# Kernel optimization log

Measured on AMD Instinct MI355X. Metric: run time of the kernel, lower is better.

The kernel has to match this reference:

```python
import jax, jax.numpy as jnp
import numpy as np

B, S, D = 256, 512, 64
LN_EPS = 1e-5


def _layernorm(x, g, b):
    mu = jnp.mean(x, axis=-1, keepdims=True)
    var = jnp.mean(jnp.square(x - mu), axis=-1, keepdims=True)
    return (x - mu) * jax.lax.rsqrt(var + LN_EPS) * g + b


def _mha(xq, xkv, in_w, in_b, out_w, out_b):
    # in_w: (3D, D) packed [Wq; Wk; Wv] as in torch nn.MultiheadAttention
    wq, wk, wv = in_w[:D], in_w[D:2 * D], in_w[2 * D:]
    bq, bk, bv = in_b[:D], in_b[D:2 * D], in_b[2 * D:]
    q = xq @ wq.T + bq      # (B, Sq, D)
    k = xkv @ wk.T + bk     # (B, Sk, D)
    v = xkv @ wv.T + bv
    scores = jnp.einsum('bqd,bkd->bqk', q, k) / jnp.sqrt(jnp.asarray(D, q.dtype))
    attn = jax.nn.softmax(scores, axis=-1)
    out = jnp.einsum('bqk,bkd->bqd', attn, v)
    return out @ out_w.T + out_b


def setup_inputs() -> dict:
    key = jax.random.key(0)
    ks = jax.random.split(key, 14)
    s = 1.0 / np.sqrt(D)
    return {
        'x_src': jax.random.normal(ks[0], (B, S), jnp.float32),
        'x_tgt': jax.random.normal(ks[1], (B, S), jnp.float32),
        'proj_w': jax.random.normal(ks[2], (D,), jnp.float32) * s,   # Linear(1, D) weight squeezed
        'proj_b': jax.random.normal(ks[3], (D,), jnp.float32) * 0.02,
        'sa_in_w': jax.random.normal(ks[4], (3 * D, D), jnp.float32) * s,
        'sa_in_b': jnp.zeros((3 * D,), jnp.float32),
        'sa_out_w': jax.random.normal(ks[5], (D, D), jnp.float32) * s,
        'sa_out_b': jnp.zeros((D,), jnp.float32),
        'sa_ln_g': jnp.ones((D,), jnp.float32),
        'sa_ln_b': jnp.zeros((D,), jnp.float32),
        'ca_in_w': jax.random.normal(ks[6], (3 * D, D), jnp.float32) * s,
        'ca_in_b': jnp.zeros((3 * D,), jnp.float32),
        'ca_out_w': jax.random.normal(ks[7], (D, D), jnp.float32) * s,
        'ca_out_b': jnp.zeros((D,), jnp.float32),
        'ca_ln_g': jnp.ones((D,), jnp.float32),
        'ca_ln_b': jnp.zeros((D,), jnp.float32),
    }


def reference(x_src, x_tgt, proj_w, proj_b,
              sa_in_w, sa_in_b, sa_out_w, sa_out_b, sa_ln_g, sa_ln_b,
              ca_in_w, ca_in_b, ca_out_w, ca_out_b, ca_ln_g, ca_ln_b):
    # Input projection: (B, S) -> (B, S, D) via Linear(1, D)
    hs = x_src[..., None] * proj_w + proj_b
    ht = x_tgt[..., None] * proj_w + proj_b
    # Shared self-attention block (pre-residual + LayerNorm), then mean pool
    zs = _layernorm(hs + _mha(hs, hs, sa_in_w, sa_in_b, sa_out_w, sa_out_b), sa_ln_g, sa_ln_b)
    zt = _layernorm(ht + _mha(ht, ht, sa_in_w, sa_in_b, sa_out_w, sa_out_b), sa_ln_g, sa_ln_b)
    z_src_private = zs.mean(axis=1)
    z_tgt_private = zt.mean(axis=1)
    # Cross-attention: Q from source, K/V from target
    zc = _layernorm(hs + _mha(hs, ht, ca_in_w, ca_in_b, ca_out_w, ca_out_b), ca_ln_g, ca_ln_b)
    z_shared = zc.mean(axis=1)
    return (z_shared, z_src_private, z_tgt_private)
```

## Files before the change

### kernel.cpp

```cpp
#include <hip/hip_runtime.h>

#define BB 256
#define SS 512
#define DD 64
#define LN_EPS 1e-5f
#define L2E 1.4426950408889634f
#define NN 16
#define PI_F 3.14159265358979f

__device__ __forceinline__ float fexp2(float x) {
#if __has_builtin(__builtin_amdgcn_exp2f)
    return __builtin_amdgcn_exp2f(x);
#else
    float r; asm("v_exp_f32 %0, %1" : "=v"(r) : "v"(x)); return r;
#endif
}

__global__ __launch_bounds__(512) void fused_kernel(
    const float* __restrict__ x_src, const float* __restrict__ x_tgt,
    const float* __restrict__ proj_w, const float* __restrict__ proj_b,
    const float* __restrict__ sa_in_w, const float* __restrict__ sa_in_b,
    const float* __restrict__ sa_out_w, const float* __restrict__ sa_out_b,
    const float* __restrict__ sa_ln_g, const float* __restrict__ sa_ln_b,
    const float* __restrict__ ca_in_w, const float* __restrict__ ca_in_b,
    const float* __restrict__ ca_out_w, const float* __restrict__ ca_out_b,
    const float* __restrict__ ca_ln_g, const float* __restrict__ ca_ln_b,
    float* __restrict__ out)
{
    const int tid  = threadIdx.x;
    const int b    = blockIdx.x / 3;
    const int task = blockIdx.x % 3;
    const float* xq_g = (task == 1) ? (x_tgt + b * SS) : (x_src + b * SS);
    const float* y_g  = (task == 0) ? (x_src + b * SS) : (x_tgt + b * SS);
    const int type    = (task == 2) ? 1 : 0;
    const float* in_w  = type ? ca_in_w  : sa_in_w;
    const float* in_b  = type ? ca_in_b  : sa_in_b;
    const float* out_w = type ? ca_out_w : sa_out_w;
    const float* out_b = type ? ca_out_b : sa_out_b;
    const float* g     = type ? ca_ln_g  : sa_ln_g;
    const float* lb    = type ? ca_ln_b  : sa_ln_b;
    const int out_base = ((task == 0) ? BB * DD : (task == 1) ? 2 * BB * DD : 0) + b * DD;

    __shared__ float sv[6][DD];
    __shared__ float cvec[3][DD];
    __shared__ float cst[8];
    __shared__ __align__(16) float ys_l[SS];
    __shared__ float rymx[8], rymn[8], rxmx[8], rxmn[8];
    __shared__ float rP[8], rT[8], rI[8];
    __shared__ float tj_l[NN];
    __shared__ __align__(16) float ac_l[NN];
    __shared__ float bc[7];

    const int wave = tid >> 6, lane = tid & 63;

    const float xq = xq_g[tid];
    const float y  = y_g[tid];
    ys_l[tid] = y;
    {
        float ymx = y, ymn = y, xmx = xq, xmn = xq;
        #pragma unroll
        for (int o = 32; o > 0; o >>= 1) {
            ymx = fmaxf(ymx, __shfl_down(ymx, o));
            ymn = fminf(ymn, __shfl_down(ymn, o));
            xmx = fmaxf(xmx, __shfl_down(xmx, o));
            xmn = fminf(xmn, __shfl_down(xmn, o));
        }
        if (lane == 0) { rymx[wave] = ymx; rymn[wave] = ymn;
                         rxmx[wave] = xmx; rxmn[wave] = xmn; }
    }

    if (tid < 384) {
        const int mat = tid >> 6, d = tid & 63;
        const int rb = mat % 3, vecsel = mat / 3;
        const float* W = in_w + (rb * DD + d) * DD;
        const float* v = vecsel ? proj_b : proj_w;
        float s = 0.f;
        #pragma unroll
        for (int e = 0; e < DD; e += 4) {
            float4 wv = *(const float4*)(W + e);
            float4 vv = *(const float4*)(v + e);
            s += wv.x * vv.x + wv.y * vv.y + wv.z * vv.z + wv.w * vv.w;
        }
        if (vecsel) s += in_b[rb * DD + d];
        sv[mat][d] = s;
    }
    __syncthreads();

    if (tid < 128) {
        const int which = tid >> 6, d = tid & 63;
        const float* W = out_w + d * DD;
        const float* v = sv[which ? 5 : 2];
        float s = 0.f;
        #pragma unroll
        for (int e = 0; e < DD; e += 4) {
            float4 wv = *(const float4*)(W + e);
            s += wv.x * v[e] + wv.y * v[e + 1] + wv.z * v[e + 2] + wv.w * v[e + 3];
        }
        if (which) cvec[2][d] = proj_b[d] + s + out_b[d];
        else       cvec[1][d] = s;
    }
    if (tid == 511) {
        float a = rymx[0], m = rymn[0], xa = rxmx[0], xm = rxmn[0];
        #pragma unroll
        for (int i = 1; i < 8; ++i) {
            a  = fmaxf(a,  rymx[i]); m  = fminf(m,  rymn[i]);
            xa = fmaxf(xa, rxmx[i]); xm = fminf(xm, rxmn[i]);
        }
        bc[0] = a; bc[1] = m; bc[2] = xa; bc[3] = xm;
    }
    __syncthreads();

    if (wave == 0) {
        auto wred = [](float x) {
            #pragma unroll
            for (int o = 32; o > 0; o >>= 1) x += __shfl_down(x, o);
            return __shfl(x, 0);
        };
        const float aq = sv[0][lane], ak = sv[1][lane], cq = sv[3][lane];
        const float pw = proj_w[lane];
        const float u  = cvec[1][lane], e = cvec[2][lane];

        const float alpha = wred(aq * ak) * 0.125f;
        const float gamma = wred(cq * ak) * 0.125f;
        const float m_pw = wred(pw) * (1.f / DD);
        const float m_u  = wred(u)  * (1.f / DD);
        const float m_e  = wred(e)  * (1.f / DD);
        const float a  = pw - m_pw;
        const float bb = u  - m_u;
        const float c  = e  - m_e;
        const float G11 = wred(a * a)   * (1.f / DD);
        const float G22 = wred(bb * bb) * (1.f / DD);
        const float G33 = wred(c * c)   * (1.f / DD);
        const float G12 = wred(a * bb)  * (1.f / DD);
        const float G13 = wred(a * c)   * (1.f / DD);
        const float G23 = wred(bb * c)  * (1.f / DD);

        cvec[0][lane] = a; cvec[1][lane] = bb; cvec[2][lane] = c;
        if (lane == 0) {
            cst[0] = alpha; cst[1] = gamma;
            cst[2] = G11; cst[3] = G22; cst[4] = G33;
            cst[5] = G12; cst[6] = G13; cst[7] = G23;
        }
    }
    __syncthreads();

    const float ymax = bc[0], ymin = bc[1];
    const float alpha = cst[0], gamma = cst[1];
    const float cA = alpha * bc[3] + gamma, cB = alpha * bc[2] + gamma;
    const float c_lo = fminf(cA, cB), c_hi = fmaxf(cA, cB);
    const float mid = 0.5f * (c_lo + c_hi);
    const float hw  = fmaxf(0.5f * (c_hi - c_lo), 1e-6f);

    {
        const int j0 = 2 * wave, j1 = j0 + 1;
        const float cj0 = mid + hw * __cosf(PI_F * (j0 + 0.5f) * (1.f / NN));
        const float cj1 = mid + hw * __cosf(PI_F * (j1 + 0.5f) * (1.f / NN));
        const float c0l = cj0 * L2E, c1l = cj1 * L2E;
        const float s0  = fmaxf(c0l * ymax, c0l * ymin);
        const float s1  = fmaxf(c1l * ymax, c1l * ymin);
        float S00 = 0.f, S10 = 0.f, S01 = 0.f, S11 = 0.f;
        #pragma unroll
        for (int i = 0; i < 8; ++i) {
            const float yv = ys_l[lane + (i << 6)];
            const float e0 = fexp2(c0l * yv - s0);
            const float e1 = fexp2(c1l * yv - s1);
            S00 += e0; S10 += yv * e0;
            S01 += e1; S11 += yv * e1;
        }
        #pragma unroll
        for (int o = 32; o > 0; o >>= 1) {
            S00 += __shfl_down(S00, o); S10 += __shfl_down(S10, o);
            S01 += __shfl_down(S01, o); S11 += __shfl_down(S11, o);
        }
        if (lane == 0) { tj_l[j0] = S10 / S00; tj_l[j1] = S11 / S01; }
    }
    __syncthreads();

    if (wave == 0 && lane < NN) {
        float acc = 0.f;
        #pragma unroll
        for (int j = 0; j < NN; ++j)
            acc += tj_l[j] * __cosf(PI_F * lane * (j + 0.5f) * (1.f / NN));
        float a = acc * (2.f / NN);
        if (lane == 0) a *= 0.5f;
        ac_l[lane] = a;
    }
    __syncthreads();

    float4 A0 = *(const float4*)&ac_l[0];
    float4 A1 = *(const float4*)&ac_l[4];
    float4 A2 = *(const float4*)&ac_l[8];
    float4 A3 = *(const float4*)&ac_l[12];
    const float a_[NN] = { A0.x, A0.y, A0.z, A0.w, A1.x, A1.y, A1.z, A1.w,
                           A2.x, A2.y, A2.z, A2.w, A3.x, A3.y, A3.z, A3.w };

    const float cq = alpha * xq + gamma;
    float xi = (cq - mid) / hw;
    xi = fminf(1.f, fmaxf(-1.f, xi));
    const float x2 = 2.f * xi;
    float b1 = 0.f, b2 = 0.f;
    #pragma unroll
    for (int k = NN - 1; k >= 1; --k) {
        const float bn = fmaf(x2, b1, a_[k] - b2);
        b2 = b1; b1 = bn;
    }
    const float t = fmaf(xi, b1, a_[0] - b2);

    const float G11 = cst[2], G22 = cst[3], G33 = cst[4];
    const float G12 = cst[5], G13 = cst[6], G23 = cst[7];
    const float var = xq * xq * G11 + t * t * G22 + G33
                    + 2.f * (xq * t * G12 + xq * G13 + t * G23);
    const float inv = rsqrtf(var + LN_EPS);

    float pP = xq * inv, pT = t * inv, pI = inv;
    #pragma unroll
    for (int o = 32; o > 0; o >>= 1) {
        pP += __shfl_down(pP, o);
        pT += __shfl_down(pT, o);
        pI += __shfl_down(pI, o);
    }
    if (lane == 0) { rP[wave] = pP; rT[wave] = pT; rI[wave] = pI; }
    __syncthreads();
    if (tid == 0) {
        float sP = 0.f, sT = 0.f, sI = 0.f;
        #pragma unroll
        for (int i = 0; i < 8; ++i) { sP += rP[i]; sT += rT[i]; sI += rI[i]; }
        bc[4] = sP * (1.f / SS); bc[5] = sT * (1.f / SS); bc[6] = sI * (1.f / SS);
    }
    __syncthreads();

    if (tid < DD) {
        const float P = bc[4], T = bc[5], I = bc[6];
        float z = (P * cvec[0][tid] + T * cvec[1][tid] + I * cvec[2][tid]) * g[tid] + lb[tid];
        out[out_base + tid] = z;
    }
}

extern "C" void kernel_launch(void* const* d_in, const int* in_sizes, int n_in,
                              void* d_out, int out_size, void* d_ws, size_t ws_size,
                              hipStream_t stream) {
    const float* x_src    = (const float*)d_in[0];
    const float* x_tgt    = (const float*)d_in[1];
    const float* proj_w   = (const float*)d_in[2];
    const float* proj_b   = (const float*)d_in[3];
    const float* sa_in_w  = (const float*)d_in[4];
    const float* sa_in_b  = (const float*)d_in[5];
    const float* sa_out_w = (const float*)d_in[6];
    const float* sa_out_b = (const float*)d_in[7];
    const float* sa_ln_g  = (const float*)d_in[8];
    const float* sa_ln_b  = (const float*)d_in[9];
    const float* ca_in_w  = (const float*)d_in[10];
    const float* ca_in_b  = (const float*)d_in[11];
    const float* ca_out_w = (const float*)d_in[12];
    const float* ca_out_b = (const float*)d_in[13];
    const float* ca_ln_g  = (const float*)d_in[14];
    const float* ca_ln_b  = (const float*)d_in[15];
    float* out = (float*)d_out;

    fused_kernel<<<BB * 3, 512, 0, stream>>>(
        x_src, x_tgt, proj_w, proj_b,
        sa_in_w, sa_in_b, sa_out_w, sa_out_b, sa_ln_g, sa_ln_b,
        ca_in_w, ca_in_b, ca_out_w, ca_out_b, ca_ln_g, ca_ln_b,
        out);
}
```

Before: 105.7 us.

## Hoist per-weight precomputation into a single-block prep kernel

The weight-only projections, out-projection vectors and Gram constants were recomputed in each of the 768 blocks. They are now computed once by a separate one-block prep kernel, written to workspace, and read by the main kernel. This removes redundant global weight reads and two block barriers per block. In exchange it adds a second serialized kernel launch, and the main kernel reads its constants from global memory instead of LDS.

```diff
diff --git a/kernel.cpp b/kernel.cpp
--- a/kernel.cpp
+++ b/kernel.cpp
@@ -8,6 +8,8 @@
 #define NN 16
 #define PI_F 3.14159265358979f
 
+#define WS_TYPE_STRIDE 256
+
 __device__ __forceinline__ float fexp2(float x) {
 #if __has_builtin(__builtin_amdgcn_exp2f)
     return __builtin_amdgcn_exp2f(x);
@@ -16,63 +18,25 @@
 #endif
 }
 
-__global__ __launch_bounds__(512) void fused_kernel(
-    const float* __restrict__ x_src, const float* __restrict__ x_tgt,
+
+__global__ __launch_bounds__(1024) void prep_kernel(
     const float* __restrict__ proj_w, const float* __restrict__ proj_b,
     const float* __restrict__ sa_in_w, const float* __restrict__ sa_in_b,
     const float* __restrict__ sa_out_w, const float* __restrict__ sa_out_b,
-    const float* __restrict__ sa_ln_g, const float* __restrict__ sa_ln_b,
     const float* __restrict__ ca_in_w, const float* __restrict__ ca_in_b,
     const float* __restrict__ ca_out_w, const float* __restrict__ ca_out_b,
-    const float* __restrict__ ca_ln_g, const float* __restrict__ ca_ln_b,
-    float* __restrict__ out)
+    float* __restrict__ ws)
 {
-    const int tid  = threadIdx.x;
-    const int b    = blockIdx.x / 3;
-    const int task = blockIdx.x % 3;
-    const float* xq_g = (task == 1) ? (x_tgt + b * SS) : (x_src + b * SS);
-    const float* y_g  = (task == 0) ? (x_src + b * SS) : (x_tgt + b * SS);
-    const int type    = (task == 2) ? 1 : 0;
-    const float* in_w  = type ? ca_in_w  : sa_in_w;
-    const float* in_b  = type ? ca_in_b  : sa_in_b;
-    const float* out_w = type ? ca_out_w : sa_out_w;
-    const float* out_b = type ? ca_out_b : sa_out_b;
-    const float* g     = type ? ca_ln_g  : sa_ln_g;
-    const float* lb    = type ? ca_ln_b  : sa_ln_b;
-    const int out_base = ((task == 0) ? BB * DD : (task == 1) ? 2 * BB * DD : 0) + b * DD;
-
-    __shared__ float sv[6][DD];
-    __shared__ float cvec[3][DD];
-    __shared__ float cst[8];
-    __shared__ __align__(16) float ys_l[SS];
-    __shared__ float rymx[8], rymn[8], rxmx[8], rxmn[8];
-    __shared__ float rP[8], rT[8], rI[8];
-    __shared__ float tj_l[NN];
-    __shared__ __align__(16) float ac_l[NN];
-    __shared__ float bc[7];
-
-    const int wave = tid >> 6, lane = tid & 63;
-
-    const float xq = xq_g[tid];
-    const float y  = y_g[tid];
-    ys_l[tid] = y;
-    {
-        float ymx = y, ymn = y, xmx = xq, xmn = xq;
-        #pragma unroll
-        for (int o = 32; o > 0; o >>= 1) {
-            ymx = fmaxf(ymx, __shfl_down(ymx, o));
-            ymn = fminf(ymn, __shfl_down(ymn, o));
-            xmx = fmaxf(xmx, __shfl_down(xmx, o));
-            xmn = fminf(xmn, __shfl_down(xmn, o));
-        }
-        if (lane == 0) { rymx[wave] = ymx; rymn[wave] = ymn;
-                         rxmx[wave] = xmx; rxmn[wave] = xmn; }
-    }
-
-    if (tid < 384) {
+    const int tid = threadIdx.x;
+    __shared__ float sv[2][6][DD];
+    __shared__ float suu[2][DD], see[2][DD];
+
+    if (tid < 768) {
         const int mat = tid >> 6, d = tid & 63;
-        const int rb = mat % 3, vecsel = mat / 3;
-        const float* W = in_w + (rb * DD + d) * DD;
+        const int type = mat / 6, which = mat % 6;
+        const int rb = which % 3;
+        const int vecsel = which / 3;
+        const float* W = (type ? ca_in_w : sa_in_w) + (rb * DD + d) * DD;
         const float* v = vecsel ? proj_b : proj_w;
         float s = 0.f;
         #pragma unroll
@@ -81,44 +45,43 @@
             float4 vv = *(const float4*)(v + e);
             s += wv.x * vv.x + wv.y * vv.y + wv.z * vv.z + wv.w * vv.w;
         }
-        if (vecsel) s += in_b[rb * DD + d];
-        sv[mat][d] = s;
-    }
-    __syncthreads();
-
-    if (tid < 128) {
-        const int which = tid >> 6, d = tid & 63;
-        const float* W = out_w + d * DD;
-        const float* v = sv[which ? 5 : 2];
+        if (vecsel) s += (type ? ca_in_b : sa_in_b)[rb * DD + d];
+        sv[type][which][d] = s;
+    }
+    __syncthreads();
+
+    if (tid < 256) {
+        const int mat = tid >> 6, d = tid & 63;
+        const int type = mat >> 1, which = mat & 1;
+        const float* W = (type ? ca_out_w : sa_out_w) + d * DD;
+        const float* v = sv[type][which ? 5 : 2];
         float s = 0.f;
         #pragma unroll
         for (int e = 0; e < DD; e += 4) {
             float4 wv = *(const float4*)(W + e);
             s += wv.x * v[e] + wv.y * v[e + 1] + wv.z * v[e + 2] + wv.w * v[e + 3];
         }
-        if (which) cvec[2][d] = proj_b[d] + s + out_b[d];
-        else       cvec[1][d] = s;
-    }
-    if (tid == 511) {
-        float a = rymx[0], m = rymn[0], xa = rxmx[0], xm = rxmn[0];
-        #pragma unroll
-        for (int i = 1; i < 8; ++i) {
-            a  = fmaxf(a,  rymx[i]); m  = fminf(m,  rymn[i]);
-            xa = fmaxf(xa, rxmx[i]); xm = fminf(xm, rxmn[i]);
-        }
-        bc[0] = a; bc[1] = m; bc[2] = xa; bc[3] = xm;
-    }
-    __syncthreads();
-
-    if (wave == 0) {
+        if (which) {
+            s += (type ? ca_out_b : sa_out_b)[d];
+            see[type][d] = proj_b[d] + s;
+        } else {
+            suu[type][d] = s;
+        }
+    }
+    __syncthreads();
+
+    const int wave = tid >> 6, lane = tid & 63;
+    if (wave < 2) {
+        const int type = wave;
         auto wred = [](float x) {
             #pragma unroll
             for (int o = 32; o > 0; o >>= 1) x += __shfl_down(x, o);
             return __shfl(x, 0);
         };
-        const float aq = sv[0][lane], ak = sv[1][lane], cq = sv[3][lane];
+        const float aq = sv[type][0][lane], ak = sv[type][1][lane];
+        const float cq = sv[type][3][lane];
         const float pw = proj_w[lane];
-        const float u  = cvec[1][lane], e = cvec[2][lane];
+        const float u  = suu[type][lane], e = see[type][lane];
 
         const float alpha = wred(aq * ak) * 0.125f;
         const float gamma = wred(cq * ak) * 0.125f;
@@ -135,17 +98,70 @@
         const float G13 = wred(a * c)   * (1.f / DD);
         const float G23 = wred(bb * c)  * (1.f / DD);
 
-        cvec[0][lane] = a; cvec[1][lane] = bb; cvec[2][lane] = c;
+        float* w = ws + type * WS_TYPE_STRIDE;
+        w[8 + lane] = a; w[72 + lane] = bb; w[136 + lane] = c;
         if (lane == 0) {
-            cst[0] = alpha; cst[1] = gamma;
-            cst[2] = G11; cst[3] = G22; cst[4] = G33;
-            cst[5] = G12; cst[6] = G13; cst[7] = G23;
-        }
+            w[0] = alpha; w[1] = gamma;
+            w[2] = G11; w[3] = G22; w[4] = G33; w[5] = G12; w[6] = G13; w[7] = G23;
+        }
+    }
+}
+
+__global__ __launch_bounds__(512) void main_kernel(
+    const float* __restrict__ x_src, const float* __restrict__ x_tgt,
+    const float* __restrict__ sa_ln_g, const float* __restrict__ sa_ln_b,
+    const float* __restrict__ ca_ln_g, const float* __restrict__ ca_ln_b,
+    const float* __restrict__ ws, float* __restrict__ out)
+{
+    const int tid  = threadIdx.x;
+    const int b    = blockIdx.x / 3;
+    const int task = blockIdx.x % 3;
+    const float* xq_g = (task == 1) ? (x_tgt + b * SS) : (x_src + b * SS);
+    const float* y_g  = (task == 0) ? (x_src + b * SS) : (x_tgt + b * SS);
+    const int type    = (task == 2) ? 1 : 0;
+    const float* w  = ws + type * WS_TYPE_STRIDE;
+    const float* g  = type ? ca_ln_g : sa_ln_g;
+    const float* lb = type ? ca_ln_b : sa_ln_b;
+    const int out_base = ((task == 0) ? BB * DD : (task == 1) ? 2 * BB * DD : 0) + b * DD;
+
+    __shared__ __align__(16) float ys_l[SS];
+    __shared__ float rymx[8], rymn[8], rxmx[8], rxmn[8];
+    __shared__ float rP[8], rT[8], rI[8];
+    __shared__ float tj_l[NN];
+    __shared__ __align__(16) float ac_l[NN];
+    __shared__ float bc[7];
+
+    const int wave = tid >> 6, lane = tid & 63;
+
+    const float xq = xq_g[tid];
+    const float y  = y_g[tid];
+    ys_l[tid] = y;
+    {
+        float ymx = y, ymn = y, xmx = xq, xmn = xq;
+        #pragma unroll
+        for (int o = 32; o > 0; o >>= 1) {
+            ymx = fmaxf(ymx, __shfl_down(ymx, o));
+            ymn = fminf(ymn, __shfl_down(ymn, o));
+            xmx = fmaxf(xmx, __shfl_down(xmx, o));
+            xmn = fminf(xmn, __shfl_down(xmn, o));
+        }
+        if (lane == 0) { rymx[wave] = ymx; rymn[wave] = ymn;
+                         rxmx[wave] = xmx; rxmn[wave] = xmn; }
+    }
+    __syncthreads();
+    if (tid == 0) {
+        float a = rymx[0], m = rymn[0], xa = rxmx[0], xm = rxmn[0];
+        #pragma unroll
+        for (int i = 1; i < 8; ++i) {
+            a  = fmaxf(a,  rymx[i]); m  = fminf(m,  rymn[i]);
+            xa = fmaxf(xa, rxmx[i]); xm = fminf(xm, rxmn[i]);
+        }
+        bc[0] = a; bc[1] = m; bc[2] = xa; bc[3] = xm;
     }
     __syncthreads();
 
     const float ymax = bc[0], ymin = bc[1];
-    const float alpha = cst[0], gamma = cst[1];
+    const float alpha = w[0], gamma = w[1];
     const float cA = alpha * bc[3] + gamma, cB = alpha * bc[2] + gamma;
     const float c_lo = fminf(cA, cB), c_hi = fmaxf(cA, cB);
     const float mid = 0.5f * (c_lo + c_hi);
@@ -206,8 +222,8 @@
     }
     const float t = fmaf(xi, b1, a_[0] - b2);
 
-    const float G11 = cst[2], G22 = cst[3], G33 = cst[4];
-    const float G12 = cst[5], G13 = cst[6], G23 = cst[7];
+    const float G11 = w[2], G22 = w[3], G33 = w[4];
+    const float G12 = w[5], G13 = w[6], G23 = w[7];
     const float var = xq * xq * G11 + t * t * G22 + G33
                     + 2.f * (xq * t * G12 + xq * G13 + t * G23);
     const float inv = rsqrtf(var + LN_EPS);
@@ -231,7 +247,7 @@
 
     if (tid < DD) {
         const float P = bc[4], T = bc[5], I = bc[6];
-        float z = (P * cvec[0][tid] + T * cvec[1][tid] + I * cvec[2][tid]) * g[tid] + lb[tid];
+        float z = (P * w[8 + tid] + T * w[72 + tid] + I * w[136 + tid]) * g[tid] + lb[tid];
         out[out_base + tid] = z;
     }
 }
@@ -255,11 +271,13 @@
     const float* ca_out_b = (const float*)d_in[13];
     const float* ca_ln_g  = (const float*)d_in[14];
     const float* ca_ln_b  = (const float*)d_in[15];
+    float* ws  = (float*)d_ws;
     float* out = (float*)d_out;
 
-    fused_kernel<<<BB * 3, 512, 0, stream>>>(
-        x_src, x_tgt, proj_w, proj_b,
-        sa_in_w, sa_in_b, sa_out_w, sa_out_b, sa_ln_g, sa_ln_b,
-        ca_in_w, ca_in_b, ca_out_w, ca_out_b, ca_ln_g, ca_ln_b,
-        out);
-}
+    prep_kernel<<<1, 1024, 0, stream>>>(proj_w, proj_b,
+                                        sa_in_w, sa_in_b, sa_out_w, sa_out_b,
+                                        ca_in_w, ca_in_b, ca_out_w, ca_out_b, ws);
+    main_kernel<<<BB * 3, 512, 0, stream>>>(x_src, x_tgt,
+                                            sa_ln_g, sa_ln_b, ca_ln_g, ca_ln_b,
+                                            ws, out);
+}
```

New measurement: 99.31 us. -6.0%, faster.

## Merge three per-batch task blocks into one block computing all tasks

Applied to the files above, without the earlier changes.

Launches one block per batch element instead of three, so each block computes self-attention for source and target and cross-attention together. The input rows and weight-derived vectors are loaded and precomputed once per batch rather than once per task, and the Chebyshev node sums, coefficient fits and reductions are batched across all three tasks. This removes redundant weight projections and halves global input loads. In exchange the grid has fewer blocks (256), which may underfill the GPU, and each block carries more serial work and register pressure.

```diff
diff --git a/kernel.cpp b/kernel.cpp
--- a/kernel.cpp
+++ b/kernel.cpp
@@ -16,7 +16,7 @@
 #endif
 }
 
-__global__ __launch_bounds__(512) void fused_kernel(
+__global__ __launch_bounds__(512) void fused_all(
     const float* __restrict__ x_src, const float* __restrict__ x_tgt,
     const float* __restrict__ proj_w, const float* __restrict__ proj_b,
     const float* __restrict__ sa_in_w, const float* __restrict__ sa_in_b,
@@ -28,51 +28,41 @@
     float* __restrict__ out)
 {
     const int tid  = threadIdx.x;
-    const int b    = blockIdx.x / 3;
-    const int task = blockIdx.x % 3;
-    const float* xq_g = (task == 1) ? (x_tgt + b * SS) : (x_src + b * SS);
-    const float* y_g  = (task == 0) ? (x_src + b * SS) : (x_tgt + b * SS);
-    const int type    = (task == 2) ? 1 : 0;
-    const float* in_w  = type ? ca_in_w  : sa_in_w;
-    const float* in_b  = type ? ca_in_b  : sa_in_b;
-    const float* out_w = type ? ca_out_w : sa_out_w;
-    const float* out_b = type ? ca_out_b : sa_out_b;
-    const float* g     = type ? ca_ln_g  : sa_ln_g;
-    const float* lb    = type ? ca_ln_b  : sa_ln_b;
-    const int out_base = ((task == 0) ? BB * DD : (task == 1) ? 2 * BB * DD : 0) + b * DD;
-
-    __shared__ float sv[6][DD];
-    __shared__ float cvec[3][DD];
-    __shared__ float cst[8];
-    __shared__ __align__(16) float ys_l[SS];
-    __shared__ float rymx[8], rymn[8], rxmx[8], rxmn[8];
-    __shared__ float rP[8], rT[8], rI[8];
-    __shared__ float tj_l[NN];
-    __shared__ __align__(16) float ac_l[NN];
-    __shared__ float bc[7];
-
+    const int b    = blockIdx.x;
     const int wave = tid >> 6, lane = tid & 63;
 
-    const float xq = xq_g[tid];
-    const float y  = y_g[tid];
-    ys_l[tid] = y;
+    __shared__ __align__(16) float xs_l[SS];
+    __shared__ __align__(16) float xt_l[SS];
+    __shared__ float sv[2][6][DD];
+    __shared__ float cw[2][3][DD];
+    __shared__ float cst[2][8];
+    __shared__ float rmx[8][4];
+    __shared__ float bb4[4];
+    __shared__ float tj_l[3 * NN];
+    __shared__ float ac_l[3 * NN];
+    __shared__ float rpti[8][9];
+    __shared__ float ptio[9];
+
+    const float xs = x_src[b * SS + tid];
+    const float xt = x_tgt[b * SS + tid];
+    xs_l[tid] = xs; xt_l[tid] = xt;
     {
-        float ymx = y, ymn = y, xmx = xq, xmn = xq;
+        float sx = xs, sn = xs, tx = xt, tn = xt;
         #pragma unroll
         for (int o = 32; o > 0; o >>= 1) {
-            ymx = fmaxf(ymx, __shfl_down(ymx, o));
-            ymn = fminf(ymn, __shfl_down(ymn, o));
-            xmx = fmaxf(xmx, __shfl_down(xmx, o));
-            xmn = fminf(xmn, __shfl_down(xmn, o));
-        }
-        if (lane == 0) { rymx[wave] = ymx; rymn[wave] = ymn;
-                         rxmx[wave] = xmx; rxmn[wave] = xmn; }
-    }
-
-    if (tid < 384) {
-        const int mat = tid >> 6, d = tid & 63;
-        const int rb = mat % 3, vecsel = mat / 3;
-        const float* W = in_w + (rb * DD + d) * DD;
+            sx = fmaxf(sx, __shfl_down(sx, o));
+            sn = fminf(sn, __shfl_down(sn, o));
+            tx = fmaxf(tx, __shfl_down(tx, o));
+            tn = fminf(tn, __shfl_down(tn, o));
+        }
+        if (lane == 0) { rmx[wave][0] = sx; rmx[wave][1] = sn;
+                         rmx[wave][2] = tx; rmx[wave][3] = tn; }
+    }
+
+    for (int m = wave; m < 12; m += 8) {
+        const int type = m / 6, which = m % 6;
+        const int rb = which % 3, vecsel = which / 3;
+        const float* W = (type ? ca_in_w : sa_in_w) + (rb * DD + lane) * DD;
         const float* v = vecsel ? proj_b : proj_w;
         float s = 0.f;
         #pragma unroll
@@ -81,44 +71,46 @@
             float4 vv = *(const float4*)(v + e);
             s += wv.x * vv.x + wv.y * vv.y + wv.z * vv.z + wv.w * vv.w;
         }
-        if (vecsel) s += in_b[rb * DD + d];
-        sv[mat][d] = s;
-    }
-    __syncthreads();
-
-    if (tid < 128) {
-        const int which = tid >> 6, d = tid & 63;
-        const float* W = out_w + d * DD;
-        const float* v = sv[which ? 5 : 2];
+        if (vecsel) s += (type ? ca_in_b : sa_in_b)[rb * DD + lane];
+        sv[type][which][lane] = s;
+    }
+    __syncthreads();
+
+    if (wave < 4) {
+        const int type = wave >> 1, which = wave & 1;
+        const float* W = (type ? ca_out_w : sa_out_w) + lane * DD;
+        const float* v = sv[type][which ? 5 : 2];
         float s = 0.f;
         #pragma unroll
         for (int e = 0; e < DD; e += 4) {
             float4 wv = *(const float4*)(W + e);
             s += wv.x * v[e] + wv.y * v[e + 1] + wv.z * v[e + 2] + wv.w * v[e + 3];
         }
-        if (which) cvec[2][d] = proj_b[d] + s + out_b[d];
-        else       cvec[1][d] = s;
+        if (which) cw[type][2][lane] = proj_b[lane] + s + (type ? ca_out_b : sa_out_b)[lane];
+        else       cw[type][1][lane] = s;
     }
     if (tid == 511) {
-        float a = rymx[0], m = rymn[0], xa = rxmx[0], xm = rxmn[0];
+        float a = rmx[0][0], m = rmx[0][1], c = rmx[0][2], d = rmx[0][3];
         #pragma unroll
         for (int i = 1; i < 8; ++i) {
-            a  = fmaxf(a,  rymx[i]); m  = fminf(m,  rymn[i]);
-            xa = fmaxf(xa, rxmx[i]); xm = fminf(xm, rxmn[i]);
-        }
-        bc[0] = a; bc[1] = m; bc[2] = xa; bc[3] = xm;
-    }
-    __syncthreads();
-
-    if (wave == 0) {
+            a = fmaxf(a, rmx[i][0]); m = fminf(m, rmx[i][1]);
+            c = fmaxf(c, rmx[i][2]); d = fminf(d, rmx[i][3]);
+        }
+        bb4[0] = a; bb4[1] = m; bb4[2] = c; bb4[3] = d;
+    }
+    __syncthreads();
+
+    if (wave < 2) {
+        const int type = wave;
         auto wred = [](float x) {
             #pragma unroll
             for (int o = 32; o > 0; o >>= 1) x += __shfl_down(x, o);
             return __shfl(x, 0);
         };
-        const float aq = sv[0][lane], ak = sv[1][lane], cq = sv[3][lane];
+        const float aq = sv[type][0][lane], ak = sv[type][1][lane];
+        const float cq = sv[type][3][lane];
         const float pw = proj_w[lane];
-        const float u  = cvec[1][lane], e = cvec[2][lane];
+        const float u  = cw[type][1][lane], e = cw[type][2][lane];
 
         const float alpha = wred(aq * ak) * 0.125f;
         const float gamma = wred(cq * ak) * 0.125f;
@@ -126,113 +118,148 @@
         const float m_u  = wred(u)  * (1.f / DD);
         const float m_e  = wred(e)  * (1.f / DD);
         const float a  = pw - m_pw;
-        const float bb = u  - m_u;
+        const float bbv = u - m_u;
         const float c  = e  - m_e;
-        const float G11 = wred(a * a)   * (1.f / DD);
-        const float G22 = wred(bb * bb) * (1.f / DD);
-        const float G33 = wred(c * c)   * (1.f / DD);
-        const float G12 = wred(a * bb)  * (1.f / DD);
-        const float G13 = wred(a * c)   * (1.f / DD);
-        const float G23 = wred(bb * c)  * (1.f / DD);
-
-        cvec[0][lane] = a; cvec[1][lane] = bb; cvec[2][lane] = c;
+        const float G11 = wred(a * a)     * (1.f / DD);
+        const float G22 = wred(bbv * bbv) * (1.f / DD);
+        const float G33 = wred(c * c)     * (1.f / DD);
+        const float G12 = wred(a * bbv)   * (1.f / DD);
+        const float G13 = wred(a * c)     * (1.f / DD);
+        const float G23 = wred(bbv * c)   * (1.f / DD);
+
+        cw[type][0][lane] = a; cw[type][1][lane] = bbv; cw[type][2][lane] = c;
         if (lane == 0) {
-            cst[0] = alpha; cst[1] = gamma;
-            cst[2] = G11; cst[3] = G22; cst[4] = G33;
-            cst[5] = G12; cst[6] = G13; cst[7] = G23;
-        }
-    }
-    __syncthreads();
-
-    const float ymax = bc[0], ymin = bc[1];
-    const float alpha = cst[0], gamma = cst[1];
-    const float cA = alpha * bc[3] + gamma, cB = alpha * bc[2] + gamma;
-    const float c_lo = fminf(cA, cB), c_hi = fmaxf(cA, cB);
-    const float mid = 0.5f * (c_lo + c_hi);
-    const float hw  = fmaxf(0.5f * (c_hi - c_lo), 1e-6f);
-
-    {
-        const int j0 = 2 * wave, j1 = j0 + 1;
-        const float cj0 = mid + hw * __cosf(PI_F * (j0 + 0.5f) * (1.f / NN));
-        const float cj1 = mid + hw * __cosf(PI_F * (j1 + 0.5f) * (1.f / NN));
+            cst[type][0] = alpha; cst[type][1] = gamma;
+            cst[type][2] = G11; cst[type][3] = G22; cst[type][4] = G33;
+            cst[type][5] = G12; cst[type][6] = G13; cst[type][7] = G23;
+        }
+    }
+    __syncthreads();
+
+    const float xsmx = bb4[0], xsmn = bb4[1], xtmx = bb4[2], xtmn = bb4[3];
+    float mid_[3], hw_[3], ymx_[3], ymn_[3];
+    #pragma unroll
+    for (int task = 0; task < 3; ++task) {
+        const int ty = (task == 2) ? 1 : 0;
+        const float al = cst[ty][0], ga = cst[ty][1];
+        const float xlo = (task == 1) ? xtmn : xsmn;
+        const float xhi = (task == 1) ? xtmx : xsmx;
+        const float cA = al * xlo + ga, cB = al * xhi + ga;
+        const float lo = fminf(cA, cB), hi = fmaxf(cA, cB);
+        mid_[task] = 0.5f * (lo + hi);
+        hw_[task]  = fmaxf(0.5f * (hi - lo), 1e-6f);
+        ymx_[task] = (task == 0) ? xsmx : xtmx;
+        ymn_[task] = (task == 0) ? xsmn : xtmn;
+    }
+
+    #pragma unroll
+    for (int p = 0; p < 3; ++p) {
+        const int n0 = 6 * wave + 2 * p, n1 = n0 + 1;
+        const int tk0 = n0 >> 4, j0 = n0 & 15;
+        const int tk1 = n1 >> 4, j1 = n1 & 15;
+        const float cj0 = mid_[tk0] + hw_[tk0] * __cosf(PI_F * (j0 + 0.5f) * (1.f / NN));
+        const float cj1 = mid_[tk1] + hw_[tk1] * __cosf(PI_F * (j1 + 0.5f) * (1.f / NN));
         const float c0l = cj0 * L2E, c1l = cj1 * L2E;
-        const float s0  = fmaxf(c0l * ymax, c0l * ymin);
-        const float s1  = fmaxf(c1l * ymax, c1l * ymin);
+        const float s0 = fmaxf(c0l * ymx_[tk0], c0l * ymn_[tk0]);
+        const float s1 = fmaxf(c1l * ymx_[tk1], c1l * ymn_[tk1]);
+        const float* y0b = (tk0 == 0) ? xs_l : xt_l;
+        const float* y1b = (tk1 == 0) ? xs_l : xt_l;
         float S00 = 0.f, S10 = 0.f, S01 = 0.f, S11 = 0.f;
         #pragma unroll
         for (int i = 0; i < 8; ++i) {
-            const float yv = ys_l[lane + (i << 6)];
-            const float e0 = fexp2(c0l * yv - s0);
-            const float e1 = fexp2(c1l * yv - s1);
-            S00 += e0; S10 += yv * e0;
-            S01 += e1; S11 += yv * e1;
+            const float ya = y0b[lane + (i << 6)];
+            const float yb = y1b[lane + (i << 6)];
+            const float e0 = fexp2(c0l * ya - s0);
+            const float e1 = fexp2(c1l * yb - s1);
+            S00 += e0; S10 += ya * e0;
+            S01 += e1; S11 += yb * e1;
         }
         #pragma unroll
         for (int o = 32; o > 0; o >>= 1) {
             S00 += __shfl_down(S00, o); S10 += __shfl_down(S10, o);
             S01 += __shfl_down(S01, o); S11 += __shfl_down(S11, o);
         }
-        if (lane == 0) { tj_l[j0] = S10 / S00; tj_l[j1] = S11 / S01; }
-    }
-    __syncthreads();
-
-    if (wave == 0 && lane < NN) {
+        if (lane == 0) { tj_l[n0] = S10 / S00; tj_l[n1] = S11 / S01; }
+    }
+    __syncthreads();
+
+    if (tid < 3 * NN) {
+        const int task = tid >> 4, k = tid & 15;
+        const float* tj = &tj_l[task * NN];
         float acc = 0.f;
         #pragma unroll
         for (int j = 0; j < NN; ++j)
-            acc += tj_l[j] * __cosf(PI_F * lane * (j + 0.5f) * (1.f / NN));
+            acc += tj[j] * __cosf(PI_F * k * (j + 0.5f) * (1.f / NN));
         float a = acc * (2.f / NN);
-        if (lane == 0) a *= 0.5f;
-        ac_l[lane] = a;
-    }
-    __syncthreads();
-
-    float4 A0 = *(const float4*)&ac_l[0];
-    float4 A1 = *(const float4*)&ac_l[4];
-    float4 A2 = *(const float4*)&ac_l[8];
-    float4 A3 = *(const float4*)&ac_l[12];
-    const float a_[NN] = { A0.x, A0.y, A0.z, A0.w, A1.x, A1.y, A1.z, A1.w,
-                           A2.x, A2.y, A2.z, A2.w, A3.x, A3.y, A3.z, A3.w };
-
-    const float cq = alpha * xq + gamma;
-    float xi = (cq - mid) / hw;
-    xi = fminf(1.f, fmaxf(-1.f, xi));
-    const float x2 = 2.f * xi;
-    float b1 = 0.f, b2 = 0.f;
+        if (k == 0) a *= 0.5f;
+        ac_l[tid] = a;
+    }
+    __syncthreads();
+
+    const float xq0 = xs, xq1 = xt, xq2 = xs;
+    float xi0 = (cst[0][0] * xq0 + cst[0][1] - mid_[0]) / hw_[0];
+    float xi1 = (cst[0][0] * xq1 + cst[0][1] - mid_[1]) / hw_[1];
+    float xi2 = (cst[1][0] * xq2 + cst[1][1] - mid_[2]) / hw_[2];
+    xi0 = fminf(1.f, fmaxf(-1.f, xi0));
+    xi1 = fminf(1.f, fmaxf(-1.f, xi1));
+    xi2 = fminf(1.f, fmaxf(-1.f, xi2));
+    const float u0 = 2.f * xi0, u1 = 2.f * xi1, u2 = 2.f * xi2;
+    float b10 = 0.f, b20 = 0.f, b11 = 0.f, b21 = 0.f, b12 = 0.f, b22 = 0.f;
     #pragma unroll
     for (int k = NN - 1; k >= 1; --k) {
-        const float bn = fmaf(x2, b1, a_[k] - b2);
-        b2 = b1; b1 = bn;
-    }
-    const float t = fmaf(xi, b1, a_[0] - b2);
-
-    const float G11 = cst[2], G22 = cst[3], G33 = cst[4];
-    const float G12 = cst[5], G13 = cst[6], G23 = cst[7];
-    const float var = xq * xq * G11 + t * t * G22 + G33
-                    + 2.f * (xq * t * G12 + xq * G13 + t * G23);
-    const float inv = rsqrtf(var + LN_EPS);
-
-    float pP = xq * inv, pT = t * inv, pI = inv;
+        const float a0 = ac_l[k], a1 = ac_l[NN + k], a2 = ac_l[2 * NN + k];
+        const float n0 = fmaf(u0, b10, a0 - b20); b20 = b10; b10 = n0;
+        const float n1 = fmaf(u1, b11, a1 - b21); b21 = b11; b11 = n1;
+        const float n2 = fmaf(u2, b12, a2 - b22); b22 = b12; b12 = n2;
+    }
+    const float t0 = fmaf(xi0, b10, ac_l[0] - b20);
+    const float t1 = fmaf(xi1, b11, ac_l[NN] - b21);
+    const float t2 = fmaf(xi2, b12, ac_l[2 * NN] - b22);
+
+    float pv[9];
+    {
+        const float* G = cst[0];
+        float var0 = xq0 * xq0 * G[2] + t0 * t0 * G[3] + G[4]
+                   + 2.f * (xq0 * t0 * G[5] + xq0 * G[6] + t0 * G[7]);
+        float var1 = xq1 * xq1 * G[2] + t1 * t1 * G[3] + G[4]
+                   + 2.f * (xq1 * t1 * G[5] + xq1 * G[6] + t1 * G[7]);
+        const float* H = cst[1];
+        float var2 = xq2 * xq2 * H[2] + t2 * t2 * H[3] + H[4]
+                   + 2.f * (xq2 * t2 * H[5] + xq2 * H[6] + t2 * H[7]);
+        const float i0 = rsqrtf(var0 + LN_EPS);
+        const float i1 = rsqrtf(var1 + LN_EPS);
+        const float i2 = rsqrtf(var2 + LN_EPS);
+        pv[0] = xq0 * i0; pv[1] = t0 * i0; pv[2] = i0;
+        pv[3] = xq1 * i1; pv[4] = t1 * i1; pv[5] = i1;
+        pv[6] = xq2 * i2; pv[7] = t2 * i2; pv[8] = i2;
+    }
     #pragma unroll
     for (int o = 32; o > 0; o >>= 1) {
-        pP += __shfl_down(pP, o);
-        pT += __shfl_down(pT, o);
-        pI += __shfl_down(pI, o);
-    }
-    if (lane == 0) { rP[wave] = pP; rT[wave] = pT; rI[wave] = pI; }
-    __syncthreads();
-    if (tid == 0) {
-        float sP = 0.f, sT = 0.f, sI = 0.f;
-        #pragma unroll
-        for (int i = 0; i < 8; ++i) { sP += rP[i]; sT += rT[i]; sI += rI[i]; }
-        bc[4] = sP * (1.f / SS); bc[5] = sT * (1.f / SS); bc[6] = sI * (1.f / SS);
-    }
-    __syncthreads();
-
-    if (tid < DD) {
-        const float P = bc[4], T = bc[5], I = bc[6];
-        float z = (P * cvec[0][tid] + T * cvec[1][tid] + I * cvec[2][tid]) * g[tid] + lb[tid];
-        out[out_base + tid] = z;
+        #pragma unroll
+        for (int q = 0; q < 9; ++q) pv[q] += __shfl_down(pv[q], o);
+    }
+    if (lane == 0) {
+        #pragma unroll
+        for (int q = 0; q < 9; ++q) rpti[wave][q] = pv[q];
+    }
+    __syncthreads();
+    if (tid < 9) {
+        float s = 0.f;
+        #pragma unroll
+        for (int i = 0; i < 8; ++i) s += rpti[i][tid];
+        ptio[tid] = s * (1.f / SS);
+    }
+    __syncthreads();
+
+    if (tid < 3 * DD) {
+        const int task = tid >> 6, d = tid & 63;
+        const int ty = (task == 2) ? 1 : 0;
+        const float P = ptio[3 * task], T = ptio[3 * task + 1], I = ptio[3 * task + 2];
+        const float* g  = ty ? ca_ln_g : sa_ln_g;
+        const float* lb = ty ? ca_ln_b : sa_ln_b;
+        const int base = (task == 0) ? BB * DD : (task == 1) ? 2 * BB * DD : 0;
+        const float z = (P * cw[ty][0][d] + T * cw[ty][1][d] + I * cw[ty][2][d]) * g[d] + lb[d];
+        out[base + b * DD + d] = z;
     }
 }
 
@@ -257,7 +284,7 @@
     const float* ca_ln_b  = (const float*)d_in[15];
     float* out = (float*)d_out;
 
-    fused_kernel<<<BB * 3, 512, 0, stream>>>(
+    fused_all<<<BB, 512, 0, stream>>>(
         x_src, x_tgt, proj_w, proj_b,
         sa_in_w, sa_in_b, sa_out_w, sa_out_b, sa_ln_g, sa_ln_b,
         ca_in_w, ca_in_b, ca_out_w, ca_out_b, ca_ln_g, ca_ln_b,
```

New measurement: 99.82 us. 1.06x faster.
